# Kernel optimization log

Hardware: AMD Instinct MI355X
Metric: run time of the kernel (lower is better)

## Reference

```python
import jax, jax.numpy as jnp
import numpy as np

B, C, H, W = 1024, 256, 16, 24
D_OUT = 256          # output_dims[1]
N_OBJ = 10           # max_num_objects (padded; ragged via objects_length)
EPS = 1e-12


def setup_inputs() -> dict:
    key = jax.random.key(0)
    ks = jax.random.split(key, 12)
    def kaiming(k, shape, fan_in):
        return jax.random.normal(k, shape, jnp.float32) * np.sqrt(2.0 / fan_in)
    inp = {
        "input": jax.random.normal(ks[0], (B, C, H, W), jnp.float32),
        "objects": jnp.zeros((B, N_OBJ, 4), jnp.int32),
        "objects_length": jax.random.randint(ks[1], (B,), 1, N_OBJ + 1).astype(jnp.int64),
        # learned query table (compute_attention uses self.query[:num_objects])
        "query": jax.random.normal(ks[2], (N_OBJ, C), jnp.float32) * 0.02,
        # 1x1 conv fuse: (C+2) -> C, stored as [C+2, C] matrix
        "conv_w": kaiming(ks[3], (C + 2, C), C + 2),
        "conv_b": jnp.zeros((C,), jnp.float32),
        "feat_w": kaiming(ks[4], (C, D_OUT), C),
        "feat_b": jnp.zeros((D_OUT,), jnp.float32),
        "obj1_w": kaiming(ks[5], (D_OUT, D_OUT), D_OUT),
        "obj1_b": jnp.zeros((D_OUT,), jnp.float32),
        "obj2_w": kaiming(ks[6], (D_OUT, D_OUT), D_OUT),
        "obj2_b": jnp.zeros((D_OUT,), jnp.float32),
    }
    return inp


def reference(input, objects, objects_length, query, conv_w, conv_b,
              feat_w, feat_b, obj1_w, obj1_b, obj2_w, obj2_b):
    b, c, h, w = input.shape
    # coord_map: x over width, y over height, each in [0,1]
    xc = jnp.linspace(0.0, 1.0, w, dtype=input.dtype)
    yc = jnp.linspace(0.0, 1.0, h, dtype=input.dtype)
    coords = jnp.stack([jnp.broadcast_to(xc[None, :], (h, w)),
                        jnp.broadcast_to(yc[:, None], (h, w))], axis=0)  # [2,H,W]
    x = jnp.concatenate([input, jnp.broadcast_to(coords[None], (b, 2, h, w))], axis=1)
    # 1x1 conv fuse + ReLU  -> [B,C,H,W]
    fused = jax.nn.relu(jnp.einsum('bchw,cd->bdhw', x, conv_w) + conv_b[None, :, None, None])
    n = query.shape[0]
    # einsum attention: scores [B,N,H,W], softmax over spatial dims
    scores = jnp.einsum('nc,bchw->bnhw', query, fused)
    attn = jax.nn.softmax(scores.reshape(b, n, h * w), axis=-1).reshape(b, n, h, w)
    # weighted sum of fused features -> object values [B,N,C]
    vals = jnp.einsum('bnhw,bchw->bnc', attn, fused)
    reps = jax.nn.relu(vals @ feat_w + feat_b)
    reps = reps / jnp.maximum(jnp.linalg.norm(reps, axis=-1, keepdims=True), EPS)
    # ragged mask: object j valid iff j < objects_length[b]
    mask = (jnp.arange(n)[None, :] < objects_length[:, None]).astype(reps.dtype)  # [B,N]
    reps = reps * mask[..., None]
    # pairwise: pair[b,i,j] = obj1(rep_i) + obj2(rep_j)
    o1 = reps @ obj1_w + obj1_b
    o2 = reps @ obj2_w + obj2_b
    pair = o1[:, :, None, :] + o2[:, None, :, :]            # [B,N,N,D]
    pair = pair * (mask[:, :, None] * mask[:, None, :])[..., None]
    return reps, pair
```

## Files before the change

kernel.cpp:

```cpp
#include <hip/hip_runtime.h>
#include <math.h>

typedef __attribute__((ext_vector_type(8))) short bf16x8;
typedef __attribute__((ext_vector_type(4))) float f32x4;

namespace {
constexpr int kB = 1024;
constexpr int kHW = 384;
constexpr int kN = 10;
constexpr int kD = 256;
}

__device__ inline void split_bf16(float x, unsigned short& hi, unsigned short& lo) {
    unsigned u = __float_as_uint(x);
    unsigned r = (u + 0x7fffu + ((u >> 16) & 1u)) & 0xffff0000u;
    hi = (unsigned short)(r >> 16);
    float res = x - __uint_as_float(r);
    unsigned u2 = __float_as_uint(res);
    lo = (unsigned short)((u2 + 0x7fffu + ((u2 >> 16) & 1u)) >> 16);
}

__device__ inline void gload16(void* lds, const void* g) {
    __builtin_amdgcn_global_load_lds((const __attribute__((address_space(1))) unsigned int*)g,
                                     (__attribute__((address_space(3))) unsigned int*)lds,
                                     16, 0, 0);
}

__global__ void wprep_kernel(const float* __restrict__ convw,
                             unsigned short* __restrict__ Whs,
                             unsigned short* __restrict__ Wls) {
    int i = blockIdx.x * 256 + threadIdx.x;
    for (; i < 65536; i += 16384) {
        int tile = i >> 12;
        int nt = tile >> 3, kstep = tile & 7;
        int rem = i & 4095;
        int n_loc = rem >> 5, i16 = rem & 31;
        int k = kstep * 32 + (i16 ^ ((n_loc & 3) << 3));
        int n = nt * 128 + n_loc;
        unsigned short h, l;
        split_bf16(convw[k * 256 + n], h, l);
        Whs[i] = h;
        Wls[i] = l;
    }
}

__global__ __launch_bounds__(256, 2)
void conv_mfma_kernel(const float* __restrict__ input,
                      const unsigned short* __restrict__ Whs,
                      const unsigned short* __restrict__ Wls,
                      const float* __restrict__ convw,
                      const float* __restrict__ convb,
                      float* __restrict__ fused) {
    __shared__ unsigned short Ah[128 * 32];
    __shared__ unsigned short Al[128 * 32];
    __shared__ unsigned short Bh[128 * 32];
    __shared__ unsigned short Bl[128 * 32];
    __shared__ float Raw[2][32 * 128];

    const int tid = threadIdx.x;
    const int lane = tid & 63;
    const int wid = tid >> 6;
    const int wr = wid >> 1, wc = wid & 1;
    const int kq = lane >> 4, lr = lane & 15;

    const int mtile = blockIdx.x >> 1;
    const int ntile = blockIdx.x & 1;
    const int b = mtile / 3;
    const int hw0 = (mtile % 3) * 128;

    const int sm = tid >> 1;
    const int skh = (tid & 1) * 16;

    f32x4 acc[4][4];
#pragma unroll
    for (int i = 0; i < 4; ++i)
#pragma unroll
        for (int j = 0; j < 4; ++j) acc[i][j] = (f32x4){0.f, 0.f, 0.f, 0.f};

    const size_t inBase = ((size_t)b * 256) * 384 + hw0;

    auto issue_raw = [&](int ks, int buf) {
#pragma unroll
        for (int rd = 0; rd < 4; ++rd) {
            int o = tid * 16 + rd * 4096;
            int r = o >> 9;
            int inb = o & 511;
            gload16((char*)&Raw[buf][0] + o,
                    (const char*)(input + inBase + (size_t)(ks * 32 + r) * 384) + inb);
        }
    };
    auto issue_B = [&](int ks) {
        const char* srcH = (const char*)(Whs + (size_t)(ntile * 8 + ks) * 4096);
        const char* srcL = (const char*)(Wls + (size_t)(ntile * 8 + ks) * 4096);
#pragma unroll
        for (int rd = 0; rd < 2; ++rd) {
            int o = tid * 16 + rd * 4096;
            gload16((char*)Bh + o, srcH + o);
            gload16((char*)Bl + o, srcL + o);
        }
    };
    auto cvt_write_A = [&](int buf) {
        float v[16];
#pragma unroll
        for (int j = 0; j < 16; ++j) v[j] = Raw[buf][(skh + j) * 128 + sm];
        unsigned hw_[8], lw_[8];
#pragma unroll
        for (int j = 0; j < 8; ++j) {
            unsigned short h0, l0, h1, l1;
            split_bf16(v[2 * j], h0, l0);
            split_bf16(v[2 * j + 1], h1, l1);
            hw_[j] = (unsigned)h0 | ((unsigned)h1 << 16);
            lw_[j] = (unsigned)l0 | ((unsigned)l1 << 16);
        }
        const int s = (sm & 3) << 4;
        char* bh = (char*)Ah + sm * 64;
        char* bl = (char*)Al + sm * 64;
        *(uint4*)(bh + (((2 * skh)) ^ s))      = make_uint4(hw_[0], hw_[1], hw_[2], hw_[3]);
        *(uint4*)(bh + (((2 * skh) + 16) ^ s)) = make_uint4(hw_[4], hw_[5], hw_[6], hw_[7]);
        *(uint4*)(bl + (((2 * skh)) ^ s))      = make_uint4(lw_[0], lw_[1], lw_[2], lw_[3]);
        *(uint4*)(bl + (((2 * skh) + 16) ^ s)) = make_uint4(lw_[4], lw_[5], lw_[6], lw_[7]);
    };

    issue_raw(0, 0);
    issue_B(0);
    __syncthreads();
    cvt_write_A(0);
    issue_raw(1, 1);
    __syncthreads();

    for (int ks = 0; ks < 8; ++ks) {
        bf16x8 afh[4], afl[4], bfh[4], bfl[4];
#pragma unroll
        for (int fm = 0; fm < 4; ++fm) {
            int m = wr * 64 + fm * 16 + lr;
            int a = m * 64 + ((16 * kq) ^ ((m & 3) << 4));
            afh[fm] = *(const bf16x8*)((const char*)Ah + a);
            afl[fm] = *(const bf16x8*)((const char*)Al + a);
        }
#pragma unroll
        for (int fn = 0; fn < 4; ++fn) {
            int n = wc * 64 + fn * 16 + lr;
            int a = n * 64 + ((16 * kq) ^ ((n & 3) << 4));
            bfh[fn] = *(const bf16x8*)((const char*)Bh + a);
            bfl[fn] = *(const bf16x8*)((const char*)Bl + a);
        }
        __syncthreads();
        if (ks < 7) {
            cvt_write_A((ks + 1) & 1);
            if (ks < 6) issue_raw(ks + 2, ks & 1);
            issue_B(ks + 1);
        }
#pragma unroll
        for (int fn = 0; fn < 4; ++fn)
#pragma unroll
            for (int fm = 0; fm < 4; ++fm) {
                acc[fm][fn] = __builtin_amdgcn_mfma_f32_16x16x32_bf16(afh[fm], bfh[fn], acc[fm][fn], 0, 0, 0);
                acc[fm][fn] = __builtin_amdgcn_mfma_f32_16x16x32_bf16(afl[fm], bfh[fn], acc[fm][fn], 0, 0, 0);
                acc[fm][fn] = __builtin_amdgcn_mfma_f32_16x16x32_bf16(afh[fm], bfl[fn], acc[fm][fn], 0, 0, 0);
            }
        if (ks < 7) __syncthreads();
    }

    float wxv[4], wyv[4], bbv[4];
#pragma unroll
    for (int fn = 0; fn < 4; ++fn) {
        int d = ntile * 128 + wc * 64 + fn * 16 + lr;
        wxv[fn] = convw[256 * 256 + d];
        wyv[fn] = convw[257 * 256 + d];
        bbv[fn] = convb[d];
    }
#pragma unroll
    for (int fm = 0; fm < 4; ++fm)
#pragma unroll
        for (int r = 0; r < 4; ++r) {
            int m = wr * 64 + fm * 16 + kq * 4 + r;
            int hw = hw0 + m;
            int row = hw / 24, col = hw % 24;
            float xc = (float)col * (1.0f / 23.0f);
            float yc = (float)row * (1.0f / 15.0f);
            size_t obase = ((size_t)b * 384 + hw) * 256;
#pragma unroll
            for (int fn = 0; fn < 4; ++fn) {
                int d = ntile * 128 + wc * 64 + fn * 16 + lr;
                float v = acc[fm][fn][r] + wxv[fn] * xc + wyv[fn] * yc + bbv[fn];
                fused[obase + d] = fmaxf(v, 0.0f);
            }
        }
}

__global__ __launch_bounds__(256, 3)
void scene_rest_kernel(const float* __restrict__ fused,
                       const int* __restrict__ lenRaw,
                       const float* __restrict__ query,
                       const float* __restrict__ featw,
                       const float* __restrict__ featb,
                       const float* __restrict__ o1w,
                       const float* __restrict__ o1b,
                       const float* __restrict__ o2w,
                       const float* __restrict__ o2b,
                       float* __restrict__ outReps,
                       float* __restrict__ outPair) {
    const int b = blockIdx.x;
    const int tid = threadIdx.x;
    const int lane = tid & 63;
    const int wv = tid >> 6;

    __shared__ float sc[kN][kHW];
    __shared__ float bufA[kN][256];
    __shared__ float bufR[kN][256];
    __shared__ float bufC[kN][256];

    const int is64 = (lenRaw[1] == 0) ? 1 : 0;
    const int len = is64 ? lenRaw[2 * b] : lenRaw[b];

    const float4* f4 = reinterpret_cast<const float4*>(fused + (size_t)b * kHW * 256);
    const float4* q4 = reinterpret_cast<const float4*>(query);
    for (int hw = wv; hw < kHW; hw += 4) {
        float4 f = f4[hw * 64 + lane];
        float p[kN];
#pragma unroll
        for (int n = 0; n < kN; ++n) {
            float4 q = q4[n * 64 + lane];
            p[n] = f.x * q.x + f.y * q.y + f.z * q.z + f.w * q.w;
        }
#pragma unroll
        for (int off = 32; off >= 1; off >>= 1)
#pragma unroll
            for (int n = 0; n < kN; ++n) p[n] += __shfl_xor(p[n], off, 64);
        if (lane == 0)
#pragma unroll
            for (int n = 0; n < kN; ++n) sc[n][hw] = p[n];
    }
    __syncthreads();

    for (int n = wv; n < kN; n += 4) {
        float v6[6];
        float m = -1e30f;
#pragma unroll
        for (int i = 0; i < 6; ++i) { v6[i] = sc[n][lane + 64 * i]; m = fmaxf(m, v6[i]); }
#pragma unroll
        for (int off = 32; off >= 1; off >>= 1) m = fmaxf(m, __shfl_xor(m, off, 64));
        float s = 0.0f;
#pragma unroll
        for (int i = 0; i < 6; ++i) { v6[i] = __expf(v6[i] - m); s += v6[i]; }
#pragma unroll
        for (int off = 32; off >= 1; off >>= 1) s += __shfl_xor(s, off, 64);
        float inv = 1.0f / s;
#pragma unroll
        for (int i = 0; i < 6; ++i) sc[n][lane + 64 * i] = v6[i] * inv;
    }
    __syncthreads();

    {
        const float* fb = fused + (size_t)b * kHW * 256;
        float va[kN];
#pragma unroll
        for (int n = 0; n < kN; ++n) va[n] = 0.0f;
        for (int hw = 0; hw < kHW; ++hw) {
            float f = fb[(size_t)hw * 256 + tid];
#pragma unroll
            for (int n = 0; n < kN; ++n) va[n] = fmaf(sc[n][hw], f, va[n]);
        }
#pragma unroll
        for (int n = 0; n < kN; ++n) bufA[n][tid] = va[n];
    }
    __syncthreads();

    {
        float ra[kN];
        float fb0 = featb[tid];
#pragma unroll
        for (int n = 0; n < kN; ++n) ra[n] = fb0;
        for (int k = 0; k < 256; ++k) {
            float w = featw[k * 256 + tid];
#pragma unroll
            for (int n = 0; n < kN; ++n) ra[n] = fmaf(bufA[n][k], w, ra[n]);
        }
#pragma unroll
        for (int n = 0; n < kN; ++n) bufR[n][tid] = fmaxf(ra[n], 0.0f);
    }
    __syncthreads();

    {
        float4* r4 = reinterpret_cast<float4*>(&bufR[0][0]);
        float4* or4 = reinterpret_cast<float4*>(outReps + (size_t)b * kN * 256);
        for (int n = wv; n < kN; n += 4) {
            float4 r = r4[n * 64 + lane];
            float ss = r.x * r.x + r.y * r.y + r.z * r.z + r.w * r.w;
#pragma unroll
            for (int off = 32; off >= 1; off >>= 1) ss += __shfl_xor(ss, off, 64);
            float norm = sqrtf(ss);
            float scale = (n < len) ? (1.0f / fmaxf(norm, 1e-12f)) : 0.0f;
            r.x *= scale; r.y *= scale; r.z *= scale; r.w *= scale;
            r4[n * 64 + lane] = r;
            or4[n * 64 + lane] = r;
        }
    }
    __syncthreads();

    {
        float a1[kN], a2[kN];
        float b1 = o1b[tid], b2 = o2b[tid];
#pragma unroll
        for (int n = 0; n < kN; ++n) { a1[n] = b1; a2[n] = b2; }
        for (int k = 0; k < 256; ++k) {
            float w1 = o1w[k * 256 + tid];
            float w2 = o2w[k * 256 + tid];
#pragma unroll
            for (int n = 0; n < kN; ++n) {
                float r = bufR[n][k];
                a1[n] = fmaf(r, w1, a1[n]);
                a2[n] = fmaf(r, w2, a2[n]);
            }
        }
#pragma unroll
        for (int n = 0; n < kN; ++n) { bufA[n][tid] = a1[n]; bufC[n][tid] = a2[n]; }
    }
    __syncthreads();

    {
        float* pb = outPair + (size_t)b * kN * kN * 256;
#pragma unroll
        for (int i = 0; i < kN; ++i) {
            float o1v = bufA[i][tid];
            bool mvalid = (i < len);
#pragma unroll
            for (int j = 0; j < kN; ++j) {
                float v = (mvalid && (j < len)) ? (o1v + bufC[j][tid]) : 0.0f;
                pb[(size_t)(i * kN + j) * 256 + tid] = v;
            }
        }
    }
}

extern "C" void kernel_launch(void* const* d_in, const int* in_sizes, int n_in,
                              void* d_out, int out_size, void* d_ws, size_t ws_size,
                              hipStream_t stream) {
    const float* input  = (const float*)d_in[0];
    const int*   lenRaw = (const int*)d_in[2];
    const float* query  = (const float*)d_in[3];
    const float* convw  = (const float*)d_in[4];
    const float* convb  = (const float*)d_in[5];
    const float* featw  = (const float*)d_in[6];
    const float* featb  = (const float*)d_in[7];
    const float* o1w    = (const float*)d_in[8];
    const float* o1b    = (const float*)d_in[9];
    const float* o2w    = (const float*)d_in[10];
    const float* o2b    = (const float*)d_in[11];

    float* fused   = (float*)d_ws;
    float* outReps = (float*)d_out;
    float* outPair = outReps + (size_t)kB * kN * kD;

    unsigned short* Whs = (unsigned short*)outPair;
    unsigned short* Wls = Whs + 65536;

    wprep_kernel<<<64, 256, 0, stream>>>(convw, Whs, Wls);
    conv_mfma_kernel<<<6144, 256, 0, stream>>>(input, Whs, Wls, convw, convb, fused);
    scene_rest_kernel<<<kB, 256, 0, stream>>>(fused, lenRaw, query, featw, featb,
                                              o1w, o1b, o2w, o2b, outReps, outPair);
}
```

Before: 1.126 ms.

## Store fused as bf16 hi/lo planes, MFMA scores, direct A-fragment loads

```diff
diff --git a/kernel.cpp b/kernel.cpp
--- a/kernel.cpp
+++ b/kernel.cpp
@@ -9,6 +9,8 @@
 constexpr int kHW = 384;
 constexpr int kN = 10;
 constexpr int kD = 256;
+constexpr int kC = 256;
+constexpr size_t kPlane = (size_t)kB * kHW * kC;
 }
 
 __device__ inline void split_bf16(float x, unsigned short& hi, unsigned short& lo) {
@@ -18,6 +20,27 @@
     float res = x - __uint_as_float(r);
     unsigned u2 = __float_as_uint(res);
     lo = (unsigned short)((u2 + 0x7fffu + ((u2 >> 16) & 1u)) >> 16);
+}
+
+__device__ inline void split2(float x0, float x1, unsigned& hi, unsigned& lo) {
+    unsigned u0 = __float_as_uint(x0), u1 = __float_as_uint(x1);
+    unsigned h0 = u0 & 0xffff0000u, h1 = u1 & 0xffff0000u;
+    float r0 = x0 - __uint_as_float(h0);
+    float r1 = x1 - __uint_as_float(h1);
+    hi = (h0 >> 16) | h1;
+    lo = (__float_as_uint(r0) >> 16) | (__float_as_uint(r1) & 0xffff0000u);
+}
+
+__device__ inline void split1(float x, unsigned short& h, unsigned short& l) {
+    unsigned u = __float_as_uint(x);
+    unsigned hb = u & 0xffff0000u;
+    h = (unsigned short)(hb >> 16);
+    float r = x - __uint_as_float(hb);
+    l = (unsigned short)(__float_as_uint(r) >> 16);
+}
+
+__device__ inline float bfval(unsigned short u) {
+    return __uint_as_float(((unsigned)u) << 16);
 }
 
 __device__ inline void gload16(void* lds, const void* g) {
@@ -44,192 +67,188 @@
     }
 }
 
-__global__ __launch_bounds__(256, 2)
+__global__ __launch_bounds__(256, 3)
 void conv_mfma_kernel(const float* __restrict__ input,
                       const unsigned short* __restrict__ Whs,
                       const unsigned short* __restrict__ Wls,
                       const float* __restrict__ convw,
                       const float* __restrict__ convb,
-                      float* __restrict__ fused) {
-    __shared__ unsigned short Ah[128 * 32];
-    __shared__ unsigned short Al[128 * 32];
-    __shared__ unsigned short Bh[128 * 32];
-    __shared__ unsigned short Bl[128 * 32];
-    __shared__ float Raw[2][32 * 128];
+                      unsigned short* __restrict__ fhi,
+                      unsigned short* __restrict__ flo) {
+    __shared__ unsigned short Bh[2][4096];
+    __shared__ unsigned short Bl[2][4096];
 
     const int tid = threadIdx.x;
-    const int lane = tid & 63;
-    const int wid = tid >> 6;
+    const int lane = tid & 63, wid = tid >> 6;
     const int wr = wid >> 1, wc = wid & 1;
     const int kq = lane >> 4, lr = lane & 15;
 
-    const int mtile = blockIdx.x >> 1;
-    const int ntile = blockIdx.x & 1;
+    const int xcd = blockIdx.x & 7;
+    const int j = blockIdx.x >> 3;
+    const int mtile = xcd * 384 + (j >> 1);
+    const int ntile = j & 1;
     const int b = mtile / 3;
     const int hw0 = (mtile % 3) * 128;
 
-    const int sm = tid >> 1;
-    const int skh = (tid & 1) * 16;
-
-    f32x4 acc[4][4];
-#pragma unroll
-    for (int i = 0; i < 4; ++i)
-#pragma unroll
-        for (int j = 0; j < 4; ++j) acc[i][j] = (f32x4){0.f, 0.f, 0.f, 0.f};
-
-    const size_t inBase = ((size_t)b * 256) * 384 + hw0;
-
-    auto issue_raw = [&](int ks, int buf) {
-#pragma unroll
-        for (int rd = 0; rd < 4; ++rd) {
-            int o = tid * 16 + rd * 4096;
-            int r = o >> 9;
-            int inb = o & 511;
-            gload16((char*)&Raw[buf][0] + o,
-                    (const char*)(input + inBase + (size_t)(ks * 32 + r) * 384) + inb);
-        }
-    };
-    auto issue_B = [&](int ks) {
-        const char* srcH = (const char*)(Whs + (size_t)(ntile * 8 + ks) * 4096);
-        const char* srcL = (const char*)(Wls + (size_t)(ntile * 8 + ks) * 4096);
+    auto issue_B = [&](int ks, int buf) {
+        const char* sh = (const char*)(Whs + (size_t)(ntile * 8 + ks) * 4096);
+        const char* sl = (const char*)(Wls + (size_t)(ntile * 8 + ks) * 4096);
 #pragma unroll
         for (int rd = 0; rd < 2; ++rd) {
             int o = tid * 16 + rd * 4096;
-            gload16((char*)Bh + o, srcH + o);
-            gload16((char*)Bl + o, srcL + o);
+            gload16((char*)&Bh[buf][0] + o, sh + o);
+            gload16((char*)&Bl[buf][0] + o, sl + o);
         }
     };
-    auto cvt_write_A = [&](int buf) {
-        float v[16];
-#pragma unroll
-        for (int j = 0; j < 16; ++j) v[j] = Raw[buf][(skh + j) * 128 + sm];
-        unsigned hw_[8], lw_[8];
-#pragma unroll
-        for (int j = 0; j < 8; ++j) {
-            unsigned short h0, l0, h1, l1;
-            split_bf16(v[2 * j], h0, l0);
-            split_bf16(v[2 * j + 1], h1, l1);
-            hw_[j] = (unsigned)h0 | ((unsigned)h1 << 16);
-            lw_[j] = (unsigned)l0 | ((unsigned)l1 << 16);
-        }
-        const int s = (sm & 3) << 4;
-        char* bh = (char*)Ah + sm * 64;
-        char* bl = (char*)Al + sm * 64;
-        *(uint4*)(bh + (((2 * skh)) ^ s))      = make_uint4(hw_[0], hw_[1], hw_[2], hw_[3]);
-        *(uint4*)(bh + (((2 * skh) + 16) ^ s)) = make_uint4(hw_[4], hw_[5], hw_[6], hw_[7]);
-        *(uint4*)(bl + (((2 * skh)) ^ s))      = make_uint4(lw_[0], lw_[1], lw_[2], lw_[3]);
-        *(uint4*)(bl + (((2 * skh) + 16) ^ s)) = make_uint4(lw_[4], lw_[5], lw_[6], lw_[7]);
-    };
-
-    issue_raw(0, 0);
-    issue_B(0);
-    __syncthreads();
-    cvt_write_A(0);
-    issue_raw(1, 1);
-    __syncthreads();
+
+    f32x4 acc[4][4];
+#pragma unroll
+    for (int i = 0; i < 4; ++i)
+#pragma unroll
+        for (int jj = 0; jj < 4; ++jj) acc[i][jj] = (f32x4){0.f, 0.f, 0.f, 0.f};
+
+    issue_B(0, 0);
+    __syncthreads();
+
+    const float* pabase = input + (size_t)b * (kC * kHW)
+                          + (size_t)(kq * 8) * kHW + hw0 + wr * 64 + lr;
 
     for (int ks = 0; ks < 8; ++ks) {
-        bf16x8 afh[4], afl[4], bfh[4], bfl[4];
+        if (ks < 7) issue_B(ks + 1, (ks + 1) & 1);
+
+        bf16x8 afh[4], afl[4];
 #pragma unroll
         for (int fm = 0; fm < 4; ++fm) {
-            int m = wr * 64 + fm * 16 + lr;
-            int a = m * 64 + ((16 * kq) ^ ((m & 3) << 4));
-            afh[fm] = *(const bf16x8*)((const char*)Ah + a);
-            afl[fm] = *(const bf16x8*)((const char*)Al + a);
-        }
+            const float* pa = pabase + (size_t)(ks * 32) * kHW + fm * 16;
+            float v[8];
+#pragma unroll
+            for (int t = 0; t < 8; ++t) v[t] = pa[(size_t)t * kHW];
+            union { unsigned u[4]; bf16x8 f; } ch, cl;
+#pragma unroll
+            for (int p = 0; p < 4; ++p) split2(v[2 * p], v[2 * p + 1], ch.u[p], cl.u[p]);
+            afh[fm] = ch.f;
+            afl[fm] = cl.f;
+        }
+
+        const int buf = ks & 1;
 #pragma unroll
         for (int fn = 0; fn < 4; ++fn) {
             int n = wc * 64 + fn * 16 + lr;
             int a = n * 64 + ((16 * kq) ^ ((n & 3) << 4));
-            bfh[fn] = *(const bf16x8*)((const char*)Bh + a);
-            bfl[fn] = *(const bf16x8*)((const char*)Bl + a);
+            bf16x8 bfh = *(const bf16x8*)((const char*)&Bh[buf][0] + a);
+            bf16x8 bfl = *(const bf16x8*)((const char*)&Bl[buf][0] + a);
+#pragma unroll
+            for (int fm = 0; fm < 4; ++fm) {
+                acc[fm][fn] = __builtin_amdgcn_mfma_f32_16x16x32_bf16(afh[fm], bfh, acc[fm][fn], 0, 0, 0);
+                acc[fm][fn] = __builtin_amdgcn_mfma_f32_16x16x32_bf16(afl[fm], bfh, acc[fm][fn], 0, 0, 0);
+                acc[fm][fn] = __builtin_amdgcn_mfma_f32_16x16x32_bf16(afh[fm], bfl, acc[fm][fn], 0, 0, 0);
+            }
         }
         __syncthreads();
-        if (ks < 7) {
-            cvt_write_A((ks + 1) & 1);
-            if (ks < 6) issue_raw(ks + 2, ks & 1);
-            issue_B(ks + 1);
-        }
-#pragma unroll
-        for (int fn = 0; fn < 4; ++fn)
-#pragma unroll
-            for (int fm = 0; fm < 4; ++fm) {
-                acc[fm][fn] = __builtin_amdgcn_mfma_f32_16x16x32_bf16(afh[fm], bfh[fn], acc[fm][fn], 0, 0, 0);
-                acc[fm][fn] = __builtin_amdgcn_mfma_f32_16x16x32_bf16(afl[fm], bfh[fn], acc[fm][fn], 0, 0, 0);
-                acc[fm][fn] = __builtin_amdgcn_mfma_f32_16x16x32_bf16(afh[fm], bfl[fn], acc[fm][fn], 0, 0, 0);
-            }
-        if (ks < 7) __syncthreads();
     }
 
     float wxv[4], wyv[4], bbv[4];
+    int dd[4];
 #pragma unroll
     for (int fn = 0; fn < 4; ++fn) {
-        int d = ntile * 128 + wc * 64 + fn * 16 + lr;
-        wxv[fn] = convw[256 * 256 + d];
-        wyv[fn] = convw[257 * 256 + d];
-        bbv[fn] = convb[d];
+        dd[fn] = ntile * 128 + wc * 64 + fn * 16 + lr;
+        wxv[fn] = convw[256 * 256 + dd[fn]];
+        wyv[fn] = convw[257 * 256 + dd[fn]];
+        bbv[fn] = convb[dd[fn]];
     }
 #pragma unroll
     for (int fm = 0; fm < 4; ++fm)
 #pragma unroll
         for (int r = 0; r < 4; ++r) {
-            int m = wr * 64 + fm * 16 + kq * 4 + r;
-            int hw = hw0 + m;
+            int hw = hw0 + wr * 64 + fm * 16 + kq * 4 + r;
             int row = hw / 24, col = hw % 24;
             float xc = (float)col * (1.0f / 23.0f);
             float yc = (float)row * (1.0f / 15.0f);
-            size_t obase = ((size_t)b * 384 + hw) * 256;
+            size_t base = ((size_t)b * kHW + hw) * 256;
 #pragma unroll
             for (int fn = 0; fn < 4; ++fn) {
-                int d = ntile * 128 + wc * 64 + fn * 16 + lr;
                 float v = acc[fm][fn][r] + wxv[fn] * xc + wyv[fn] * yc + bbv[fn];
-                fused[obase + d] = fmaxf(v, 0.0f);
+                v = fmaxf(v, 0.0f);
+                unsigned short h, l;
+                split1(v, h, l);
+                fhi[base + dd[fn]] = h;
+                flo[base + dd[fn]] = l;
             }
         }
 }
 
 __global__ __launch_bounds__(256, 3)
-void scene_rest_kernel(const float* __restrict__ fused,
-                       const int* __restrict__ lenRaw,
-                       const float* __restrict__ query,
-                       const float* __restrict__ featw,
-                       const float* __restrict__ featb,
-                       const float* __restrict__ o1w,
-                       const float* __restrict__ o1b,
-                       const float* __restrict__ o2w,
-                       const float* __restrict__ o2b,
-                       float* __restrict__ outReps,
-                       float* __restrict__ outPair) {
-    const int b = blockIdx.x;
-    const int tid = threadIdx.x;
-    const int lane = tid & 63;
-    const int wv = tid >> 6;
-
-    __shared__ float sc[kN][kHW];
-    __shared__ float bufA[kN][256];
-    __shared__ float bufR[kN][256];
-    __shared__ float bufC[kN][256];
+void scene_kernel(const unsigned short* __restrict__ fhi,
+                  const unsigned short* __restrict__ flo,
+                  const int* __restrict__ lenRaw,
+                  const float* __restrict__ query,
+                  const float* __restrict__ featw,
+                  const float* __restrict__ featb,
+                  const float* __restrict__ o1w,
+                  const float* __restrict__ o1b,
+                  const float* __restrict__ o2w,
+                  const float* __restrict__ o2b,
+                  float* __restrict__ outReps,
+                  float* __restrict__ outPair) {
+    __shared__ float sc[kN][388];
+    __shared__ __align__(16) char U[30720];
+
+    const int b = blockIdx.x, tid = threadIdx.x;
+    const int lane = tid & 63, wv = tid >> 6;
+    const int kq = lane >> 4, lr = lane & 15;
 
     const int is64 = (lenRaw[1] == 0) ? 1 : 0;
     const int len = is64 ? lenRaw[2 * b] : lenRaw[b];
 
-    const float4* f4 = reinterpret_cast<const float4*>(fused + (size_t)b * kHW * 256);
-    const float4* q4 = reinterpret_cast<const float4*>(query);
-    for (int hw = wv; hw < kHW; hw += 4) {
-        float4 f = f4[hw * 64 + lane];
-        float p[kN];
-#pragma unroll
-        for (int n = 0; n < kN; ++n) {
-            float4 q = q4[n * 64 + lane];
-            p[n] = f.x * q.x + f.y * q.y + f.z * q.z + f.w * q.w;
-        }
-#pragma unroll
-        for (int off = 32; off >= 1; off >>= 1)
-#pragma unroll
-            for (int n = 0; n < kN; ++n) p[n] += __shfl_xor(p[n], off, 64);
-        if (lane == 0)
-#pragma unroll
-            for (int n = 0; n < kN; ++n) sc[n][hw] = p[n];
+    {
+        uint4* qh_f = (uint4*)U;
+        uint4* ql_f = (uint4*)(U + 8192);
+        for (int e = tid; e < 512; e += 256) {
+            int ks = e >> 6, l = e & 63;
+            int kq_ = (l >> 4) & 3, n = l & 15;
+            uint4 H = make_uint4(0, 0, 0, 0), L = make_uint4(0, 0, 0, 0);
+            if (n < kN) {
+                const float* qp = query + n * 256 + ks * 32 + kq_ * 8;
+                unsigned h[4], lo_[4];
+#pragma unroll
+                for (int p = 0; p < 4; ++p) split2(qp[2 * p], qp[2 * p + 1], h[p], lo_[p]);
+                H = make_uint4(h[0], h[1], h[2], h[3]);
+                L = make_uint4(lo_[0], lo_[1], lo_[2], lo_[3]);
+            }
+            qh_f[e] = H;
+            ql_f[e] = L;
+        }
+    }
+    __syncthreads();
+
+    {
+        const uint4* qh_f = (const uint4*)U;
+        const uint4* ql_f = (const uint4*)(U + 8192);
+        f32x4 acc[6];
+#pragma unroll
+        for (int i = 0; i < 6; ++i) acc[i] = (f32x4){0.f, 0.f, 0.f, 0.f};
+        const unsigned short* pah = fhi + ((size_t)b * kHW + wv * 96 + lr) * 256 + kq * 8;
+        const unsigned short* pal = flo + ((size_t)b * kHW + wv * 96 + lr) * 256 + kq * 8;
+        for (int ks = 0; ks < 8; ++ks) {
+            union { uint4 u; bf16x8 f; } qh, ql;
+            qh.u = qh_f[ks * 64 + lane];
+            ql.u = ql_f[ks * 64 + lane];
+#pragma unroll
+            for (int fm = 0; fm < 6; ++fm) {
+                bf16x8 ah = *(const bf16x8*)(pah + (size_t)fm * 16 * 256 + ks * 32);
+                bf16x8 al = *(const bf16x8*)(pal + (size_t)fm * 16 * 256 + ks * 32);
+                acc[fm] = __builtin_amdgcn_mfma_f32_16x16x32_bf16(ah, qh.f, acc[fm], 0, 0, 0);
+                acc[fm] = __builtin_amdgcn_mfma_f32_16x16x32_bf16(al, qh.f, acc[fm], 0, 0, 0);
+                acc[fm] = __builtin_amdgcn_mfma_f32_16x16x32_bf16(ah, ql.f, acc[fm], 0, 0, 0);
+            }
+        }
+        if (lr < kN) {
+#pragma unroll
+            for (int fm = 0; fm < 6; ++fm)
+#pragma unroll
+                for (int r = 0; r < 4; ++r)
+                    sc[lr][wv * 96 + fm * 16 + kq * 4 + r] = acc[fm][r];
+        }
     }
     __syncthreads();
 
@@ -252,19 +271,31 @@
     __syncthreads();
 
     {
-        const float* fb = fused + (size_t)b * kHW * 256;
         float va[kN];
 #pragma unroll
         for (int n = 0; n < kN; ++n) va[n] = 0.0f;
-        for (int hw = 0; hw < kHW; ++hw) {
-            float f = fb[(size_t)hw * 256 + tid];
-#pragma unroll
-            for (int n = 0; n < kN; ++n) va[n] = fmaf(sc[n][hw], f, va[n]);
-        }
-#pragma unroll
-        for (int n = 0; n < kN; ++n) bufA[n][tid] = va[n];
-    }
-    __syncthreads();
+        const unsigned short* ph = fhi + (size_t)b * kHW * 256 + tid;
+        const unsigned short* pl = flo + (size_t)b * kHW * 256 + tid;
+        for (int h4 = 0; h4 < kHW; h4 += 4) {
+            float f0 = bfval(ph[(size_t)(h4 + 0) * 256]) + bfval(pl[(size_t)(h4 + 0) * 256]);
+            float f1 = bfval(ph[(size_t)(h4 + 1) * 256]) + bfval(pl[(size_t)(h4 + 1) * 256]);
+            float f2 = bfval(ph[(size_t)(h4 + 2) * 256]) + bfval(pl[(size_t)(h4 + 2) * 256]);
+            float f3 = bfval(ph[(size_t)(h4 + 3) * 256]) + bfval(pl[(size_t)(h4 + 3) * 256]);
+#pragma unroll
+            for (int n = 0; n < kN; ++n) {
+                float4 a4 = *(const float4*)&sc[n][h4];
+                va[n] = fmaf(a4.x, f0, fmaf(a4.y, f1, fmaf(a4.z, f2, fmaf(a4.w, f3, va[n]))));
+            }
+        }
+        float* bufA = (float*)U;
+#pragma unroll
+        for (int n = 0; n < kN; ++n) bufA[n * 256 + tid] = va[n];
+    }
+    __syncthreads();
+
+    float* bufA = (float*)U;
+    float* bufR = (float*)(U + 10240);
+    float* bufC = (float*)(U + 20480);
 
     {
         float ra[kN];
@@ -274,15 +305,15 @@
         for (int k = 0; k < 256; ++k) {
             float w = featw[k * 256 + tid];
 #pragma unroll
-            for (int n = 0; n < kN; ++n) ra[n] = fmaf(bufA[n][k], w, ra[n]);
-        }
-#pragma unroll
-        for (int n = 0; n < kN; ++n) bufR[n][tid] = fmaxf(ra[n], 0.0f);
-    }
-    __syncthreads();
-
-    {
-        float4* r4 = reinterpret_cast<float4*>(&bufR[0][0]);
+            for (int n = 0; n < kN; ++n) ra[n] = fmaf(bufA[n * 256 + k], w, ra[n]);
+        }
+#pragma unroll
+        for (int n = 0; n < kN; ++n) bufR[n * 256 + tid] = fmaxf(ra[n], 0.0f);
+    }
+    __syncthreads();
+
+    {
+        float4* r4 = reinterpret_cast<float4*>(bufR);
         float4* or4 = reinterpret_cast<float4*>(outReps + (size_t)b * kN * 256);
         for (int n = wv; n < kN; n += 4) {
             float4 r = r4[n * 64 + lane];
@@ -308,13 +339,13 @@
             float w2 = o2w[k * 256 + tid];
 #pragma unroll
             for (int n = 0; n < kN; ++n) {
-                float r = bufR[n][k];
+                float r = bufR[n * 256 + k];
                 a1[n] = fmaf(r, w1, a1[n]);
                 a2[n] = fmaf(r, w2, a2[n]);
             }
         }
 #pragma unroll
-        for (int n = 0; n < kN; ++n) { bufA[n][tid] = a1[n]; bufC[n][tid] = a2[n]; }
+        for (int n = 0; n < kN; ++n) { bufA[n * 256 + tid] = a1[n]; bufC[n * 256 + tid] = a2[n]; }
     }
     __syncthreads();
 
@@ -322,12 +353,12 @@
         float* pb = outPair + (size_t)b * kN * kN * 256;
 #pragma unroll
         for (int i = 0; i < kN; ++i) {
-            float o1v = bufA[i][tid];
+            float o1v = bufA[i * 256 + tid];
             bool mvalid = (i < len);
 #pragma unroll
-            for (int j = 0; j < kN; ++j) {
-                float v = (mvalid && (j < len)) ? (o1v + bufC[j][tid]) : 0.0f;
-                pb[(size_t)(i * kN + j) * 256 + tid] = v;
+            for (int jo = 0; jo < kN; ++jo) {
+                float v = (mvalid && (jo < len)) ? (o1v + bufC[jo * 256 + tid]) : 0.0f;
+                pb[(size_t)(i * kN + jo) * 256 + tid] = v;
             }
         }
     }
@@ -348,7 +379,8 @@
     const float* o2w    = (const float*)d_in[10];
     const float* o2b    = (const float*)d_in[11];
 
-    float* fused   = (float*)d_ws;
+    unsigned short* fhi = (unsigned short*)d_ws;
+    unsigned short* flo = fhi + kPlane;
     float* outReps = (float*)d_out;
     float* outPair = outReps + (size_t)kB * kN * kD;
 
@@ -356,7 +388,7 @@
     unsigned short* Wls = Whs + 65536;
 
     wprep_kernel<<<64, 256, 0, stream>>>(convw, Whs, Wls);
-    conv_mfma_kernel<<<6144, 256, 0, stream>>>(input, Whs, Wls, convw, convb, fused);
-    scene_rest_kernel<<<kB, 256, 0, stream>>>(fused, lenRaw, query, featw, featb,
-                                              o1w, o1b, o2w, o2b, outReps, outPair);
-}
+    conv_mfma_kernel<<<6144, 256, 0, stream>>>(input, Whs, Wls, convw, convb, fhi, flo);
+    scene_kernel<<<kB, 256, 0, stream>>>(fhi, flo, lenRaw, query, featw, featb,
+                                         o1w, o1b, o2w, o2b, outReps, outPair);
+}
```

After: 1.018 ms. 9.6% less time.
